# Optimization experiments

Hardware: AMD Instinct MI355X
Metric: run time of the kernel (lower is better)

Reference implementation:

```python
import jax, jax.numpy as jnp
import numpy as np


def _exp_levels(dx, depth):
    """Tensor-algebra exponential of a single increment dx [B, C]:
    level j is dx^{(x) j} / j!, flattened to [B, C^j]."""
    B = dx.shape[0]
    levels = [dx]
    for j in range(2, depth + 1):
        levels.append((jnp.einsum('bi,bj->bij', levels[-1], dx) / j).reshape(B, -1))
    return levels


def _chen_step(levels, dx, depth):
    """Chen's identity: sig(path * segment) = sig(path) (x) exp(dx).
    levels: tuple of [B, C^k] for k=1..depth. dx: [B, C]."""
    B = dx.shape[0]
    exps = _exp_levels(dx, depth)
    new = []
    for k in range(1, depth + 1):
        acc = levels[k - 1] + exps[k - 1]  # A_k * 1  +  1 * E_k
        for j in range(1, k):
            # A_{k-j} (x) E_j, flattened: [B, C^{k-j}] x [B, C^j] -> [B, C^k]
            acc = acc + jnp.einsum('bi,bj->bij', levels[k - j - 1], exps[j - 1]).reshape(B, -1)
        new.append(acc)
    return tuple(new)


def setup_inputs() -> dict:
    key = jax.random.key(0)
    path = jax.random.normal(key, (64, 512, 10), dtype=jnp.float32)
    return {"path": path, "depth": 4}


def reference(path, depth):
    # signature(path, depth, stream=False, basepoint=False, inverse=False,
    #           initial=None, scalar_term=False)
    dx = path[:, 1:] - path[:, :-1]  # [B, L-1, C] increments
    B = path.shape[0]
    # Initialise with the signature of the first segment: exp(dx_0).
    init = tuple(_exp_levels(dx[:, 0], depth))
    # Fold remaining segments via Chen's relation (a sequential scan; the
    # original's batch-trick is just a reassociation of this same product).
    dx_rest = jnp.swapaxes(dx[:, 1:], 0, 1)  # [L-2, B, C]

    def step(carry, d):
        return _chen_step(carry, d, depth), None

    carry, _ = jax.lax.scan(step, init, dx_rest)
    # Concatenate levels: output [B, C + C^2 + ... + C^depth]
    return jnp.concatenate(carry, axis=-1)
```

## Files before the change

### kernel.cpp

```cpp
#include <hip/hip_runtime.h>


#define CH      10
#define NSTEPS  511
#define ROW     12
#define SIGSZ   11110

__global__ __launch_bounds__(256, 1)
void sig_kernel(const float* __restrict__ path, float* __restrict__ out) {
    __shared__ __align__(16) float dxL[NSTEPS * ROW];

    const int tid  = threadIdx.x;
    const int b    = blockIdx.x >> 2;
    const int part = blockIdx.x & 3;

    const float* p = path + b * (512 * CH);
    for (int e = tid; e < NSTEPS * CH; e += 256) {
        int s = e / CH;
        int c = e - s * CH;
        dxL[s * ROW + c] = p[e + CH] - p[e];
    }
    __syncthreads();

    const int id = part * 256 + tid;
    if (id < 1000) {
        const int ci = id / 100;
        const int cj = (id / 10) % 10;
        const int ck = id % 10;

        float a1 = 0.f, a2 = 0.f, a3 = 0.f;
        float a4[10];
        #pragma unroll
        for (int l = 0; l < 10; ++l) a4[l] = 0.f;

        #pragma unroll 4
        for (int s = 0; s < NSTEPS; ++s) {
            const float* row = dxL + s * ROW;
            const float4 d0 = *(const float4*)(row);
            const float4 d1 = *(const float4*)(row + 4);
            const float2 d2 = *(const float2*)(row + 8);
            const float dxi = row[ci];
            const float dxj = row[cj];
            const float dxk = row[ck];

            const float p1 = a1 * (1.f / 6.f)  + dxi * (1.f / 24.f);
            const float q1 = a1 * 0.5f         + dxi * (1.f / 6.f);
            const float r1 = a1                + dxi * 0.5f;
            const float p2 = a2 * 0.5f + p1 * dxj;
            const float q2 = a2        + q1 * dxj;
            a2 += r1 * dxj;
            const float p3 = a3 + p2 * dxk;
            a3 += q2 * dxk;
            a1 += dxi;

            a4[0] += p3 * d0.x; a4[1] += p3 * d0.y;
            a4[2] += p3 * d0.z; a4[3] += p3 * d0.w;
            a4[4] += p3 * d1.x; a4[5] += p3 * d1.y;
            a4[6] += p3 * d1.z; a4[7] += p3 * d1.w;
            a4[8] += p3 * d2.x; a4[9] += p3 * d2.y;
        }

        float* ob = out + b * SIGSZ;
        float* o4 = ob + 1110 + id * 10;
        #pragma unroll
        for (int l = 0; l < 10; ++l) o4[l] = a4[l];
        ob[110 + id] = a3;
        if (ck == 0)            ob[10 + ci * 10 + cj] = a2;
        if (ck == 0 && cj == 0) ob[ci] = a1;
    }
}

extern "C" void kernel_launch(void* const* d_in, const int* in_sizes, int n_in,
                              void* d_out, int out_size, void* d_ws, size_t ws_size,
                              hipStream_t stream) {
    const float* path = (const float*)d_in[0];
    float* out = (float*)d_out;
    sig_kernel<<<dim3(256), dim3(256), 0, stream>>>(path, out);
}
```

Before: 102.1 us.

## Split signature scan into parallel time-chunks combined via Chen's identity

The 511-step sequential scan is split into 8 groups of 64 steps. A separate kernel computes the increments into a padded workspace, and a group kernel computes each chunk's partial signature across 8x more blocks. A combine kernel then folds the 8 partial signatures per batch with the truncated tensor product. This is meant to remove the long serial dependency chain and the low occupancy of one block per batch-part. In exchange it adds two extra launches and roughly 23 MB of workspace traffic for the partial signatures.

```diff
diff --git a/kernel.cpp b/kernel.cpp
--- a/kernel.cpp
+++ b/kernel.cpp
@@ -1,65 +1,144 @@
 #include <hip/hip_runtime.h>
 
 
-#define CH      10
-#define NSTEPS  511
-#define ROW     12
-#define SIGSZ   11110
+#define CH     10
+#define LEN    512
+#define NB     64
+#define NSTEP  511
+#define ROWF   12
+#define GROUPS 8
+#define SPG    64
+#define SIGSZ  11110
+#define TSTR   68
+#define DXG_FLOATS (NB * LEN * ROWF)
 
-__global__ __launch_bounds__(256, 1)
-void sig_kernel(const float* __restrict__ path, float* __restrict__ out) {
-    __shared__ __align__(16) float dxL[NSTEPS * ROW];
+__global__ void dx_kernel(const float* __restrict__ path, float* __restrict__ dxg) {
+    int idx = blockIdx.x * blockDim.x + threadIdx.x;
+    const int total = NB * LEN * ROWF;
+    for (int e = idx; e < total; e += gridDim.x * blockDim.x) {
+        int c   = e % ROWF;
+        int row = e / ROWF;
+        int s   = row % LEN;
+        float v = 0.f;
+        if (c < CH && s < NSTEP) {
+            const float* p = path + row * CH + c;
+            v = p[CH] - p[0];
+        }
+        dxg[e] = v;
+    }
+}
 
+__global__ __launch_bounds__(256, 6)
+void sig_group_kernel(const float* __restrict__ dxg, float* __restrict__ wsig) {
+    __shared__ __align__(16) float dxT[CH * TSTR];
     const int tid  = threadIdx.x;
-    const int b    = blockIdx.x >> 2;
+    const int b    = blockIdx.x >> 5;
+    const int g    = (blockIdx.x >> 2) & 7;
     const int part = blockIdx.x & 3;
 
-    const float* p = path + b * (512 * CH);
-    for (int e = tid; e < NSTEPS * CH; e += 256) {
+    const float* drows = dxg + (b * LEN + g * SPG) * ROWF;
+
+    for (int e = tid; e < CH * SPG; e += 256) {
         int s = e / CH;
         int c = e - s * CH;
-        dxL[s * ROW + c] = p[e + CH] - p[e];
+        dxT[c * TSTR + s] = drows[s * ROWF + c];
     }
     __syncthreads();
 
     const int id = part * 256 + tid;
     if (id < 1000) {
-        const int ci = id / 100;
-        const int cj = (id / 10) % 10;
-        const int ck = id % 10;
-
-        float a1 = 0.f, a2 = 0.f, a3 = 0.f;
-        float a4[10];
+        const int ci = id / 100, cj = (id / 10) % 10, ck = id % 10;
+        float a1 = 0.f, a2 = 0.f, a3 = 0.f, a4[10];
         #pragma unroll
         for (int l = 0; l < 10; ++l) a4[l] = 0.f;
 
-        #pragma unroll 4
-        for (int s = 0; s < NSTEPS; ++s) {
-            const float* row = dxL + s * ROW;
-            const float4 d0 = *(const float4*)(row);
-            const float4 d1 = *(const float4*)(row + 4);
-            const float2 d2 = *(const float2*)(row + 8);
-            const float dxi = row[ci];
-            const float dxj = row[cj];
-            const float dxk = row[ck];
+        for (int s = 0; s < SPG; s += 4) {
+            const float4 di = *(const float4*)(dxT + ci * TSTR + s);
+            const float4 dj = *(const float4*)(dxT + cj * TSTR + s);
+            const float4 dk = *(const float4*)(dxT + ck * TSTR + s);
+            #pragma unroll
+            for (int u = 0; u < 4; ++u) {
+                const float* row = drows + (s + u) * ROWF;
+                const float r0 = row[0], r1 = row[1], r2 = row[2], r3 = row[3];
+                const float r4 = row[4], r5 = row[5], r6 = row[6], r7 = row[7];
+                const float r8 = row[8], r9 = row[9];
+                const float dxi = (&di.x)[u];
+                const float dxj = (&dj.x)[u];
+                const float dxk = (&dk.x)[u];
 
-            const float p1 = a1 * (1.f / 6.f)  + dxi * (1.f / 24.f);
-            const float q1 = a1 * 0.5f         + dxi * (1.f / 6.f);
-            const float r1 = a1                + dxi * 0.5f;
-            const float p2 = a2 * 0.5f + p1 * dxj;
-            const float q2 = a2        + q1 * dxj;
-            a2 += r1 * dxj;
-            const float p3 = a3 + p2 * dxk;
-            a3 += q2 * dxk;
-            a1 += dxi;
+                const float p1 = a1 * (1.f / 6.f) + dxi * (1.f / 24.f);
+                const float q1 = a1 * 0.5f        + dxi * (1.f / 6.f);
+                const float rr = a1               + dxi * 0.5f;
+                const float p2 = a2 * 0.5f + p1 * dxj;
+                const float q2 = a2        + q1 * dxj;
+                a2 += rr * dxj;
+                const float p3 = a3 + p2 * dxk;
+                a3 += q2 * dxk;
+                a1 += dxi;
 
-            a4[0] += p3 * d0.x; a4[1] += p3 * d0.y;
-            a4[2] += p3 * d0.z; a4[3] += p3 * d0.w;
-            a4[4] += p3 * d1.x; a4[5] += p3 * d1.y;
-            a4[6] += p3 * d1.z; a4[7] += p3 * d1.w;
-            a4[8] += p3 * d2.x; a4[9] += p3 * d2.y;
+                a4[0] += p3 * r0; a4[1] += p3 * r1;
+                a4[2] += p3 * r2; a4[3] += p3 * r3;
+                a4[4] += p3 * r4; a4[5] += p3 * r5;
+                a4[6] += p3 * r6; a4[7] += p3 * r7;
+                a4[8] += p3 * r8; a4[9] += p3 * r9;
+            }
         }
 
+        float* wb = wsig + (b * GROUPS + g) * SIGSZ;
+        float* w4 = wb + 1110 + id * 10;
+        #pragma unroll
+        for (int l = 0; l < 10; ++l) w4[l] = a4[l];
+        wb[110 + id] = a3;
+        if (ck == 0)            wb[10 + ci * 10 + cj] = a2;
+        if (ck == 0 && cj == 0) wb[ci] = a1;
+    }
+}
+
+__global__ __launch_bounds__(256, 1)
+void combine_kernel(const float* __restrict__ wsig, float* __restrict__ out) {
+    __shared__ float Bs[1110];
+    const int tid  = threadIdx.x;
+    const int b    = blockIdx.x >> 2;
+    const int part = blockIdx.x & 3;
+    const int id   = part * 256 + tid;
+    const bool active = id < 1000;
+    const int ci = id / 100, cj = (id / 10) % 10, ck = id % 10;
+
+    const float* w0 = wsig + (b * GROUPS) * SIGSZ;
+    float a1 = 0.f, a2 = 0.f, a3 = 0.f, a4[10];
+    #pragma unroll
+    for (int l = 0; l < 10; ++l) a4[l] = 0.f;
+    if (active) {
+        a1 = w0[ci];
+        a2 = w0[10 + ci * 10 + cj];
+        a3 = w0[110 + id];
+        #pragma unroll
+        for (int l = 0; l < 10; ++l) a4[l] = w0[1110 + id * 10 + l];
+    }
+
+    for (int g = 1; g < GROUPS; ++g) {
+        const float* wg = w0 + g * SIGSZ;
+        __syncthreads();
+        for (int e = tid; e < 1110; e += 256) Bs[e] = wg[e];
+        __syncthreads();
+        if (active) {
+            float b4[10];
+            #pragma unroll
+            for (int l = 0; l < 10; ++l) b4[l] = wg[1110 + id * 10 + l];
+            const float* B1 = Bs;
+            const float* B2 = Bs + 10;
+            const float* B3 = Bs + 110;
+            #pragma unroll
+            for (int l = 0; l < 10; ++l)
+                a4[l] += a3 * B1[l] + a2 * B2[ck * 10 + l]
+                       + a1 * B3[(cj * 10 + ck) * 10 + l] + b4[l];
+            a3 += a2 * B1[ck] + a1 * B2[cj * 10 + ck] + B3[(ci * 10 + cj) * 10 + ck];
+            a2 += a1 * B1[cj] + B2[ci * 10 + cj];
+            a1 += B1[ci];
+        }
+    }
+
+    if (active) {
         float* ob = out + b * SIGSZ;
         float* o4 = ob + 1110 + id * 10;
         #pragma unroll
@@ -74,6 +153,11 @@
                               void* d_out, int out_size, void* d_ws, size_t ws_size,
                               hipStream_t stream) {
     const float* path = (const float*)d_in[0];
-    float* out = (float*)d_out;
-    sig_kernel<<<dim3(256), dim3(256), 0, stream>>>(path, out);
+    float* out  = (float*)d_out;
+    float* dxg  = (float*)d_ws;
+    float* wsig = dxg + DXG_FLOATS;
+
+    dx_kernel<<<dim3(1536), dim3(256), 0, stream>>>(path, dxg);
+    sig_group_kernel<<<dim3(NB * GROUPS * 4), dim3(256), 0, stream>>>(dxg, wsig);
+    combine_kernel<<<dim3(NB * 4), dim3(256), 0, stream>>>(wsig, out);
 }
```

Result: no change. 103.6 us (+1.5%).

## Split time axis into groups and combine partial signatures via Chen products

Applied to the files above, without the earlier changes.

Splits the 511-step sequential scan into 8 groups of 64 steps per batch. Each group computes its own partial signature in a separate block, with each thread owning an (i,j) pair and holding 110 accumulators in registers. A second kernel folds the 8 partial signatures with Chen's identity. This shortens the serial dependency chain and raises the block count, at the cost of a workspace round trip, an extra launch and heavy register pressure (28 threads duplicate work).

```diff
diff --git a/kernel.cpp b/kernel.cpp
--- a/kernel.cpp
+++ b/kernel.cpp
@@ -1,79 +1,162 @@
 #include <hip/hip_runtime.h>
 
 
-#define CH      10
-#define NSTEPS  511
-#define ROW     12
-#define SIGSZ   11110
+#define CH     10
+#define LEN    512
+#define NB     64
+#define GROUPS 8
+#define SPG    64
+#define SIGSZ  11110
+#define SIGW   11112
+#define L4W    1112
+#define TSTR   68
 
-__global__ __launch_bounds__(256, 1)
-void sig_kernel(const float* __restrict__ path, float* __restrict__ out) {
-    __shared__ __align__(16) float dxL[NSTEPS * ROW];
+__global__ __launch_bounds__(128, 1)
+void sig_group_kernel(const float* __restrict__ path, float* __restrict__ wsig) {
+    __shared__ __align__(16) float rowL[SPG * 12];
+    __shared__ __align__(16) float dxT[CH * TSTR];
+    const int tid = threadIdx.x;
+    const int b   = blockIdx.x >> 3;
+    const int g   = blockIdx.x & 7;
+    const int s0  = g * SPG;
 
-    const int tid  = threadIdx.x;
-    const int b    = blockIdx.x >> 2;
-    const int part = blockIdx.x & 3;
-
-    const float* p = path + b * (512 * CH);
-    for (int e = tid; e < NSTEPS * CH; e += 256) {
-        int s = e / CH;
-        int c = e - s * CH;
-        dxL[s * ROW + c] = p[e + CH] - p[e];
+    const float* __restrict__ pb = path + b * (LEN * CH);
+    for (int e = tid; e < SPG * CH; e += 128) {
+        int s = e / CH, c = e - s * CH;
+        int gs = s0 + s;
+        const float* p = pb + gs * CH + c;
+        float nxt = p[(gs < LEN - 1) ? CH : 0];
+        float v = (gs < LEN - 1) ? (nxt - p[0]) : 0.f;
+        rowL[s * 12 + c] = v;
+        dxT[c * TSTR + s] = v;
     }
     __syncthreads();
 
-    const int id = part * 256 + tid;
-    if (id < 1000) {
-        const int ci = id / 100;
-        const int cj = (id / 10) % 10;
-        const int ck = id % 10;
+    const int ij = (tid < 100) ? tid : tid - 28;
+    const int i = ij / 10, j = ij % 10;
 
-        float a1 = 0.f, a2 = 0.f, a3 = 0.f;
-        float a4[10];
+    float a1 = 0.f, a2 = 0.f, a3[10], a4[100];
+    #pragma unroll
+    for (int k = 0; k < 10; ++k) a3[k] = 0.f;
+    #pragma unroll
+    for (int m = 0; m < 100; ++m) a4[m] = 0.f;
+
+    for (int s4 = 0; s4 < SPG; s4 += 4) {
+        const float4 di4 = *(const float4*)(dxT + i * TSTR + s4);
+        const float4 dj4 = *(const float4*)(dxT + j * TSTR + s4);
         #pragma unroll
-        for (int l = 0; l < 10; ++l) a4[l] = 0.f;
+        for (int u = 0; u < 4; ++u) {
+            const float* row = rowL + (s4 + u) * 12;
+            const float4 ra = *(const float4*)(row);
+            const float4 rb = *(const float4*)(row + 4);
+            const float2 rc = *(const float2*)(row + 8);
+            const float r_[10] = {ra.x, ra.y, ra.z, ra.w,
+                                  rb.x, rb.y, rb.z, rb.w, rc.x, rc.y};
+            const float dxi = (&di4.x)[u];
+            const float dxj = (&dj4.x)[u];
 
-        #pragma unroll 4
-        for (int s = 0; s < NSTEPS; ++s) {
-            const float* row = dxL + s * ROW;
-            const float4 d0 = *(const float4*)(row);
-            const float4 d1 = *(const float4*)(row + 4);
-            const float2 d2 = *(const float2*)(row + 8);
-            const float dxi = row[ci];
-            const float dxj = row[cj];
-            const float dxk = row[ck];
-
-            const float p1 = a1 * (1.f / 6.f)  + dxi * (1.f / 24.f);
-            const float q1 = a1 * 0.5f         + dxi * (1.f / 6.f);
-            const float r1 = a1                + dxi * 0.5f;
-            const float p2 = a2 * 0.5f + p1 * dxj;
-            const float q2 = a2        + q1 * dxj;
-            a2 += r1 * dxj;
-            const float p3 = a3 + p2 * dxk;
-            a3 += q2 * dxk;
+            const float p1 = fmaf(dxi, 1.f / 24.f, a1 * (1.f / 6.f));
+            const float q1 = fmaf(dxi, 1.f / 6.f,  a1 * 0.5f);
+            const float rr = fmaf(dxi, 0.5f, a1);
+            const float p2 = fmaf(p1, dxj, a2 * 0.5f);
+            const float q2 = fmaf(q1, dxj, a2);
+            a2 = fmaf(rr, dxj, a2);
             a1 += dxi;
 
-            a4[0] += p3 * d0.x; a4[1] += p3 * d0.y;
-            a4[2] += p3 * d0.z; a4[3] += p3 * d0.w;
-            a4[4] += p3 * d1.x; a4[5] += p3 * d1.y;
-            a4[6] += p3 * d1.z; a4[7] += p3 * d1.w;
-            a4[8] += p3 * d2.x; a4[9] += p3 * d2.y;
+            #pragma unroll
+            for (int k = 0; k < 10; ++k) {
+                const float p3 = fmaf(p2, r_[k], a3[k]);
+                a3[k] = fmaf(q2, r_[k], a3[k]);
+                #pragma unroll
+                for (int l = 0; l < 10; ++l)
+                    a4[k * 10 + l] = fmaf(p3, r_[l], a4[k * 10 + l]);
+            }
         }
+    }
 
-        float* ob = out + b * SIGSZ;
-        float* o4 = ob + 1110 + id * 10;
+    float* wb = wsig + (b * GROUPS + g) * SIGW;
+    float4* w4 = (float4*)(wb + L4W + ij * 100);
+    #pragma unroll
+    for (int m = 0; m < 25; ++m)
+        w4[m] = make_float4(a4[4 * m], a4[4 * m + 1], a4[4 * m + 2], a4[4 * m + 3]);
+    #pragma unroll
+    for (int k = 0; k < 10; ++k) wb[110 + ij * 10 + k] = a3[k];
+    wb[10 + ij] = a2;
+    if (j == 0) wb[i] = a1;
+}
+
+__global__ __launch_bounds__(128, 1)
+void combine_kernel(const float* __restrict__ wsig, float* __restrict__ out) {
+    __shared__ float Bs[1110];
+    const int tid = threadIdx.x;
+    const int b   = blockIdx.x;
+    const int ij  = (tid < 100) ? tid : tid - 28;
+    const int i = ij / 10, j = ij % 10;
+
+    const float* __restrict__ w0 = wsig + b * GROUPS * SIGW;
+    float a1 = w0[i];
+    float a2 = w0[10 + ij];
+    float a3[10], a4[100];
+    #pragma unroll
+    for (int k = 0; k < 10; ++k) a3[k] = w0[110 + ij * 10 + k];
+    {
+        const float4* p4 = (const float4*)(w0 + L4W + ij * 100);
         #pragma unroll
-        for (int l = 0; l < 10; ++l) o4[l] = a4[l];
-        ob[110 + id] = a3;
-        if (ck == 0)            ob[10 + ci * 10 + cj] = a2;
-        if (ck == 0 && cj == 0) ob[ci] = a1;
+        for (int m = 0; m < 25; ++m) {
+            float4 v = p4[m];
+            a4[4 * m] = v.x; a4[4 * m + 1] = v.y;
+            a4[4 * m + 2] = v.z; a4[4 * m + 3] = v.w;
+        }
     }
+
+    for (int g = 1; g < GROUPS; ++g) {
+        const float* __restrict__ wg = w0 + g * SIGW;
+        __syncthreads();
+        for (int e = tid; e < 1110; e += 128) Bs[e] = wg[e];
+        __syncthreads();
+        float b4[100];
+        const float4* b4p = (const float4*)(wg + L4W + ij * 100);
+        #pragma unroll
+        for (int m = 0; m < 25; ++m) {
+            float4 v = b4p[m];
+            b4[4 * m] = v.x; b4[4 * m + 1] = v.y;
+            b4[4 * m + 2] = v.z; b4[4 * m + 3] = v.w;
+        }
+        const float* B1 = Bs;
+        const float* B2 = Bs + 10;
+        const float* B3 = Bs + 110;
+        #pragma unroll
+        for (int k = 0; k < 10; ++k) {
+            #pragma unroll
+            for (int l = 0; l < 10; ++l)
+                a4[k * 10 + l] += a3[k] * B1[l] + a2 * B2[k * 10 + l]
+                                + a1 * B3[(j * 10 + k) * 10 + l] + b4[k * 10 + l];
+        }
+        #pragma unroll
+        for (int k = 0; k < 10; ++k)
+            a3[k] += a2 * B1[k] + a1 * B2[j * 10 + k] + B3[ij * 10 + k];
+        a2 += a1 * B1[j] + B2[ij];
+        a1 += B1[i];
+    }
+
+    float* ob = out + b * SIGSZ;
+    float2* o4 = (float2*)(ob + 1110 + ij * 100);
+    #pragma unroll
+    for (int m = 0; m < 50; ++m)
+        o4[m] = make_float2(a4[2 * m], a4[2 * m + 1]);
+    #pragma unroll
+    for (int k = 0; k < 10; ++k) ob[110 + ij * 10 + k] = a3[k];
+    ob[10 + ij] = a2;
+    if (j == 0) ob[i] = a1;
 }
 
 extern "C" void kernel_launch(void* const* d_in, const int* in_sizes, int n_in,
                               void* d_out, int out_size, void* d_ws, size_t ws_size,
                               hipStream_t stream) {
     const float* path = (const float*)d_in[0];
-    float* out = (float*)d_out;
-    sig_kernel<<<dim3(256), dim3(256), 0, stream>>>(path, out);
+    float* out  = (float*)d_out;
+    float* wsig = (float*)d_ws;
+
+    sig_group_kernel<<<dim3(NB * GROUPS), dim3(128), 0, stream>>>(path, wsig);
+    combine_kernel<<<dim3(NB), dim3(128), 0, stream>>>(wsig, out);
 }
```

Result: slower. 116.9 us (+14.5%).
